# Kernel tuning notes

Measured on AMD Instinct MI355X. Metric: run time of the kernel, lower is better.

The kernel has to match this reference:

```python
import jax, jax.numpy as jnp
import numpy as np

MODEL_DIM = 1024
TOTAL_DIM = 1024
N_HEADS = 16
HEAD_DIM = TOTAL_DIM // N_HEADS


def setup_inputs() -> dict:
    key = jax.random.key(0)
    k1, k2, k3 = jax.random.split(key, 3)
    query = jax.random.normal(k1, (2, 2048, MODEL_DIM), dtype=jnp.float32)
    # nn.Linear(model_dim, 3*total_dim, bias=False): store as [in, out] for x @ W
    W_in = jax.random.normal(k2, (MODEL_DIM, 3 * TOTAL_DIM), dtype=jnp.float32) / np.sqrt(MODEL_DIM)
    W_out = jax.random.normal(k3, (TOTAL_DIM, MODEL_DIM), dtype=jnp.float32) / np.sqrt(TOTAL_DIM)
    return {"query": query, "W_in": W_in, "W_out": W_out}


def reference(query, W_in, W_out):
    B, S, _ = query.shape
    qkv = query @ W_in                      # [B, S, 3*D]
    q, k, v = jnp.split(qkv, 3, axis=-1)    # each [B, S, D]

    def to_heads(t):
        return t.reshape(B, S, N_HEADS, HEAD_DIM).transpose(0, 2, 1, 3)  # [B,H,S,d]

    q, k, v = to_heads(q), to_heads(k), to_heads(v)
    scale = 1.0 / np.sqrt(HEAD_DIM).astype(np.float32)
    scores = jnp.einsum('bhqd,bhkd->bhqk', q, k) * scale  # [B,H,S,S]
    causal = jnp.tril(jnp.ones((S, S), dtype=bool))
    scores = jnp.where(causal, scores, jnp.finfo(scores.dtype).min)
    probs = jax.nn.softmax(scores, axis=-1)
    attn = jnp.einsum('bhqk,bhkd->bhqd', probs, v)        # [B,H,S,d]
    attn = attn.transpose(0, 2, 1, 3).reshape(B, S, TOTAL_DIM)
    return attn @ W_out                     # [B, S, model_dim]
```

## Files before the change

### kernel.cpp

```cpp
#include <hip/hip_runtime.h>


typedef __bf16 bf16x8 __attribute__((ext_vector_type(8)));
typedef float f32x4 __attribute__((ext_vector_type(4)));
typedef int i32x4 __attribute__((ext_vector_type(4)));

#define B_   2
#define S_   2048
#define DM   1024
#define NH   16
#define HD   64
#define N3   3072
#define M_   4096

#define SCALE_LOG2E 0.180336884f

__device__ __forceinline__ unsigned short f2bf(float f) {
  unsigned int u = __float_as_uint(f);
  u += 0x7fffu + ((u >> 16) & 1u);
  return (unsigned short)(u >> 16);
}

__device__ __forceinline__ void gload_lds16(void* lds, const void* g) {
  __builtin_amdgcn_global_load_lds(
      (__attribute__((address_space(1))) void*)g,
      (__attribute__((address_space(3))) void*)lds, 16, 0, 0);
}

__global__ __launch_bounds__(256) void f32_to_bf16_vec(
    const float4* __restrict__ in, unsigned short* __restrict__ out, int n4) {
  int i = blockIdx.x * 256 + threadIdx.x;
  if (i < n4) {
    float4 v = in[i];
    ushort4 o;
    o.x = f2bf(v.x); o.y = f2bf(v.y); o.z = f2bf(v.z); o.w = f2bf(v.w);
    *(ushort4*)(&out[(size_t)i * 4]) = o;
  }
}

__global__ __launch_bounds__(256) void transpose_f32_bf16(
    const float* __restrict__ in, unsigned short* __restrict__ out, int R, int C) {
  __shared__ float tile[32][33];
  const int tx = threadIdx.x, ty = threadIdx.y;
  const int x = blockIdx.x * 32 + tx;
  const int y0 = blockIdx.y * 32;
#pragma unroll
  for (int j = 0; j < 32; j += 8)
    tile[ty + j][tx] = in[(size_t)(y0 + ty + j) * C + x];
  __syncthreads();
  const int ox = y0 + tx;
  const int oy0 = blockIdx.x * 32;
#pragma unroll
  for (int j = 0; j < 32; j += 8)
    out[(size_t)(oy0 + ty + j) * R + ox] = f2bf(tile[tx][ty + j]);
}

__global__ __launch_bounds__(256) void transpose_v(
    const unsigned short* __restrict__ qkv, unsigned short* __restrict__ vT) {
  __shared__ unsigned short tile[32][33];
  const int tx = threadIdx.x, ty = threadIdx.y;
  const int c0 = blockIdx.x * 32;
  const int r0 = blockIdx.y * 32;
#pragma unroll
  for (int j = 0; j < 32; j += 8)
    tile[ty + j][tx] = qkv[(size_t)(r0 + ty + j) * N3 + 2 * DM + c0 + tx];
  __syncthreads();
  const int b = r0 >> 11;
  const int srow = (r0 & 2047);
  const int head = c0 >> 6;
#pragma unroll
  for (int j = 0; j < 32; j += 8) {
    const int d = (c0 & 63) + ty + j;
    vT[(size_t)((b * NH + head) * HD + d) * S_ + srow + tx] = tile[tx][ty + j];
  }
}

template <int OUT_BF16>
__global__ __launch_bounds__(256) void gemm_abt(
    const unsigned short* __restrict__ A, const unsigned short* __restrict__ Bt,
    void* __restrict__ Cv, int M, int N, int K) {
  __shared__ __align__(16) unsigned short a_sm[128 * 32];
  __shared__ __align__(16) unsigned short b_sm[128 * 32];
  const int tid = threadIdx.x;
  const int lane = tid & 63, wave = tid >> 6;
  const int quad = lane >> 4, l15 = lane & 15;
  const int row0 = blockIdx.y * 128, col0 = blockIdx.x * 128;
  const int wm = (wave >> 1) * 64, wn = (wave & 1) * 64;

  f32x4 acc[4][4];
#pragma unroll
  for (int i = 0; i < 4; i++)
#pragma unroll
    for (int j = 0; j < 4; j++) acc[i][j] = (f32x4){0.f, 0.f, 0.f, 0.f};

  const int e0 = tid * 8;

  for (int k0 = 0; k0 < K; k0 += 32) {
    __syncthreads();
#pragma unroll
    for (int i = 0; i < 2; i++) {
      int e = e0 + i * 2048;
      int r = e >> 5, c = e & 31;
      gload_lds16(&a_sm[e], &A[(size_t)(row0 + r) * K + k0 + c]);
      gload_lds16(&b_sm[e], &Bt[(size_t)(col0 + r) * K + k0 + c]);
    }
    __syncthreads();

    bf16x8 af[4], bfb[4];
#pragma unroll
    for (int i = 0; i < 4; i++) {
      af[i]  = *(const bf16x8*)&a_sm[(wm + i * 16 + l15) * 32 + quad * 8];
      bfb[i] = *(const bf16x8*)&b_sm[(wn + i * 16 + l15) * 32 + quad * 8];
    }
#pragma unroll
    for (int i = 0; i < 4; i++)
#pragma unroll
      for (int j = 0; j < 4; j++)
        acc[i][j] = __builtin_amdgcn_mfma_f32_16x16x32_bf16(af[i], bfb[j], acc[i][j], 0, 0, 0);
  }

#pragma unroll
  for (int i = 0; i < 4; i++) {
#pragma unroll
    for (int j = 0; j < 4; j++) {
#pragma unroll
      for (int r = 0; r < 4; r++) {
        const int row = row0 + wm + i * 16 + quad * 4 + r;
        const int col = col0 + wn + j * 16 + l15;
        const float v = acc[i][j][r];
        if (OUT_BF16)
          ((unsigned short*)Cv)[(size_t)row * N + col] = f2bf(v);
        else
          ((float*)Cv)[(size_t)row * N + col] = v;
      }
    }
  }
}

__global__ __launch_bounds__(512, 4) void attn_fused3(
    const unsigned short* __restrict__ qkv,
    const unsigned short* __restrict__ vT,
    unsigned short* __restrict__ attnout) {
  const int h = blockIdx.y, b = blockIdx.z;
  const int qt = (b == 0) ? blockIdx.x : (15 - blockIdx.x);
  const int tid = threadIdx.x;
  const int lane = tid & 63, wave = tid >> 6;
  const int quad = lane >> 4, l15 = lane & 15;
  const int sw = l15 & 7;

  __shared__ __align__(16) unsigned short k_sm[2 * 4096];
  __shared__ __align__(16) unsigned short vt_sm[2 * 4096];

  const int Q0 = qt * 128;
  const int qrow = Q0 + wave * 16 + l15;
  const int wrow0 = Q0 + wave * 16;

  bf16x8 qf[2];
  {
    const unsigned short* qp = qkv + (size_t)(b * S_ + qrow) * N3 + h * HD + quad * 8;
    qf[0] = *(const bf16x8*)qp;
    qf[1] = *(const bf16x8*)(qp + 32);
  }

  f32x4 o[4];
#pragma unroll
  for (int n = 0; n < 4; n++) o[n] = (f32x4){0.f, 0.f, 0.f, 0.f};
  float lsum = 0.f;

  const int r0s = tid >> 3;
  const int gch = ((tid & 7) ^ (r0s & 7)) * 8;
  const unsigned short* kgb = qkv + (size_t)(b * S_ + r0s) * N3 + DM + h * HD + gch;
  const unsigned short* vgb = vT + (size_t)((b * NH + h) * HD + r0s) * S_ + gch;

  const int addrA = (((quad * 2) & 3) * 16 + l15) * 4;
  const int addrB = (((quad * 2 + 1) & 3) * 16 + l15) * 4;

  const int nt = 2 * qt + 2;
  gload_lds16(&k_sm[tid * 8], kgb);
  gload_lds16(&vt_sm[tid * 8], vgb);

  for (int t = 0; t < nt; t++) {
    __syncthreads();
    if (t + 1 < nt) {
      const int nb = ((t + 1) & 1) * 4096;
      gload_lds16(&k_sm[nb + tid * 8], kgb + (size_t)(t + 1) * 64 * N3);
      gload_lds16(&vt_sm[nb + tid * 8], vgb + (t + 1) * 64);
    }
    if (t * 64 > wrow0 + 15) continue;

    const unsigned short* kb = &k_sm[(t & 1) * 4096];
    const unsigned short* vb = &vt_sm[(t & 1) * 4096];

    f32x4 s[4];
#pragma unroll
    for (int mb = 0; mb < 4; mb++) s[mb] = (f32x4){0.f, 0.f, 0.f, 0.f};
#pragma unroll
    for (int mb = 0; mb < 4; mb++) {
      const int ro = (mb * 16 + l15) * 64;
      bf16x8 kf0 = *(const bf16x8*)&kb[ro + ((quad ^ sw) << 3)];
      bf16x8 kf1 = *(const bf16x8*)&kb[ro + (((4 + quad) ^ sw) << 3)];
      s[mb] = __builtin_amdgcn_mfma_f32_16x16x32_bf16(kf0, qf[0], s[mb], 0, 0, 0);
      s[mb] = __builtin_amdgcn_mfma_f32_16x16x32_bf16(kf1, qf[1], s[mb], 0, 0, 0);
    }

    if (t * 64 + 63 <= wrow0) {
#pragma unroll
      for (int mb = 0; mb < 4; mb++)
#pragma unroll
        for (int r = 0; r < 4; r++)
          s[mb][r] = exp2f(s[mb][r] * SCALE_LOG2E);
    } else {
      const int kb0 = t * 64 + quad * 4;
#pragma unroll
      for (int mb = 0; mb < 4; mb++)
#pragma unroll
        for (int r = 0; r < 4; r++) {
          const float e = exp2f(s[mb][r] * SCALE_LOG2E);
          s[mb][r] = (kb0 + mb * 16 + r <= qrow) ? e : 0.f;
        }
    }
#pragma unroll
    for (int mb = 0; mb < 4; mb++)
      lsum += (s[mb][0] + s[mb][1]) + (s[mb][2] + s[mb][3]);

    int pk[4][2];
#pragma unroll
    for (int mb = 0; mb < 4; mb++) {
      const unsigned u0 = __float_as_uint(s[mb][0]) + 0x8000u;
      const unsigned u1 = __float_as_uint(s[mb][1]) + 0x8000u;
      const unsigned u2 = __float_as_uint(s[mb][2]) + 0x8000u;
      const unsigned u3 = __float_as_uint(s[mb][3]) + 0x8000u;
      pk[mb][0] = (int)__builtin_amdgcn_perm(u1, u0, 0x07060302u);
      pk[mb][1] = (int)__builtin_amdgcn_perm(u3, u2, 0x07060302u);
    }

    const bool hi = quad >= 2;
#pragma unroll
    for (int ks = 0; ks < 2; ks++) {
      const int m0 = 2 * ks, m1 = m0 + 1;
      const int f0a = __builtin_amdgcn_ds_bpermute(addrA, pk[m0][0]);
      const int f0b = __builtin_amdgcn_ds_bpermute(addrA, pk[m1][0]);
      const int f1a = __builtin_amdgcn_ds_bpermute(addrA, pk[m0][1]);
      const int f1b = __builtin_amdgcn_ds_bpermute(addrA, pk[m1][1]);
      const int f2a = __builtin_amdgcn_ds_bpermute(addrB, pk[m0][0]);
      const int f2b = __builtin_amdgcn_ds_bpermute(addrB, pk[m1][0]);
      const int f3a = __builtin_amdgcn_ds_bpermute(addrB, pk[m0][1]);
      const int f3b = __builtin_amdgcn_ds_bpermute(addrB, pk[m1][1]);
      i32x4 fr;
      fr.x = hi ? f0b : f0a;
      fr.y = hi ? f1b : f1a;
      fr.z = hi ? f2b : f2a;
      fr.w = hi ? f3b : f3a;
      const bf16x8 pfrag = __builtin_bit_cast(bf16x8, fr);
#pragma unroll
      for (int mb = 0; mb < 4; mb++) {
        const int ro = (mb * 16 + l15) * 64;
        bf16x8 vf = *(const bf16x8*)&vb[ro + (((ks * 4 + quad) ^ sw) << 3)];
        o[mb] = __builtin_amdgcn_mfma_f32_16x16x32_bf16(vf, pfrag, o[mb], 0, 0, 0);
      }
    }
  }

  float l = lsum;
  l += __shfl_xor(l, 16);
  l += __shfl_xor(l, 32);
  const float inv = 1.0f / l;
  const size_t grow = (size_t)(b * S_ + qrow);
#pragma unroll
  for (int mb = 0; mb < 4; mb++) {
    ushort4 w;
    w.x = f2bf(o[mb][0] * inv);
    w.y = f2bf(o[mb][1] * inv);
    w.z = f2bf(o[mb][2] * inv);
    w.w = f2bf(o[mb][3] * inv);
    *(ushort4*)&attnout[grow * DM + h * HD + mb * 16 + quad * 4] = w;
  }
}

extern "C" void kernel_launch(void* const* d_in, const int* in_sizes, int n_in,
                              void* d_out, int out_size, void* d_ws, size_t ws_size,
                              hipStream_t stream) {
  const float* query = (const float*)d_in[0];
  const float* w_in  = (const float*)d_in[1];
  const float* w_out = (const float*)d_in[2];
  float* out = (float*)d_out;

  char* ws = (char*)d_ws;
  unsigned short* qbf     = (unsigned short*)(ws);
  unsigned short* vT      = (unsigned short*)(ws);
  unsigned short* w_in_t  = (unsigned short*)(ws + 8388608);
  unsigned short* w_out_t = (unsigned short*)(ws + 14680064);
  unsigned short* qkv     = (unsigned short*)(ws + 16777216);
  unsigned short* attn    = (unsigned short*)(ws + 41943040);

  f32_to_bf16_vec<<<dim3(M_ * DM / 1024), dim3(256), 0, stream>>>(
      (const float4*)query, qbf, M_ * DM / 4);
  transpose_f32_bf16<<<dim3(N3 / 32, DM / 32), dim3(32, 8), 0, stream>>>(w_in, w_in_t, DM, N3);
  transpose_f32_bf16<<<dim3(DM / 32, DM / 32), dim3(32, 8), 0, stream>>>(w_out, w_out_t, DM, DM);
  gemm_abt<1><<<dim3(N3 / 128, M_ / 128), dim3(256), 0, stream>>>(qbf, w_in_t, qkv, M_, N3, DM);
  transpose_v<<<dim3(DM / 32, M_ / 32), dim3(32, 8), 0, stream>>>(qkv, vT);
  attn_fused3<<<dim3(S_ / 128, NH, B_), dim3(512), 0, stream>>>(qkv, vT, attn);
  gemm_abt<0><<<dim3(DM / 128, M_ / 128), dim3(256), 0, stream>>>(attn, w_out_t, out, M_, DM, DM);
}
```

Baseline: 203.5 us.

## Fuse V transpose into QKV GEMM, shrink attention tiles, retile output GEMM

The QKV projection GEMM now writes Q/K into a 2048-wide buffer and emits V directly in transposed per-head layout by swapping MFMA operands, which removes the separate transpose_v kernel. It also uses a K-step of 64 with XOR-swizzled LDS and an XCD-aware block-to-tile mapping. Attention moves to 256-thread blocks over 64-row query tiles, which doubles the grid and drops the per-wave causal skip. The output GEMM gets a 128x64 tile for more blocks. The changes target a kernel launch, extra traffic for V, and low occupancy, at the cost of more K/V reloads in attention.

```diff
diff --git a/kernel.cpp b/kernel.cpp
--- a/kernel.cpp
+++ b/kernel.cpp
@@ -55,109 +55,123 @@
     out[(size_t)(oy0 + ty + j) * R + ox] = f2bf(tile[tx][ty + j]);
 }
 
-__global__ __launch_bounds__(256) void transpose_v(
-    const unsigned short* __restrict__ qkv, unsigned short* __restrict__ vT) {
-  __shared__ unsigned short tile[32][33];
-  const int tx = threadIdx.x, ty = threadIdx.y;
-  const int c0 = blockIdx.x * 32;
-  const int r0 = blockIdx.y * 32;
-#pragma unroll
-  for (int j = 0; j < 32; j += 8)
-    tile[ty + j][tx] = qkv[(size_t)(r0 + ty + j) * N3 + 2 * DM + c0 + tx];
-  __syncthreads();
-  const int b = r0 >> 11;
-  const int srow = (r0 & 2047);
-  const int head = c0 >> 6;
-#pragma unroll
-  for (int j = 0; j < 32; j += 8) {
-    const int d = (c0 & 63) + ty + j;
-    vT[(size_t)((b * NH + head) * HD + d) * S_ + srow + tx] = tile[tx][ty + j];
-  }
-}
-
-template <int OUT_BF16>
-__global__ __launch_bounds__(256) void gemm_abt(
-    const unsigned short* __restrict__ A, const unsigned short* __restrict__ Bt,
-    void* __restrict__ Cv, int M, int N, int K) {
-  __shared__ __align__(16) unsigned short a_sm[128 * 32];
-  __shared__ __align__(16) unsigned short b_sm[128 * 32];
-  const int tid = threadIdx.x;
-  const int lane = tid & 63, wave = tid >> 6;
-  const int quad = lane >> 4, l15 = lane & 15;
-  const int row0 = blockIdx.y * 128, col0 = blockIdx.x * 128;
-  const int wm = (wave >> 1) * 64, wn = (wave & 1) * 64;
-
-  f32x4 acc[4][4];
-#pragma unroll
-  for (int i = 0; i < 4; i++)
-#pragma unroll
-    for (int j = 0; j < 4; j++) acc[i][j] = (f32x4){0.f, 0.f, 0.f, 0.f};
-
-  const int e0 = tid * 8;
-
-  for (int k0 = 0; k0 < K; k0 += 32) {
-    __syncthreads();
-#pragma unroll
-    for (int i = 0; i < 2; i++) {
-      int e = e0 + i * 2048;
-      int r = e >> 5, c = e & 31;
-      gload_lds16(&a_sm[e], &A[(size_t)(row0 + r) * K + k0 + c]);
-      gload_lds16(&b_sm[e], &Bt[(size_t)(col0 + r) * K + k0 + c]);
-    }
-    __syncthreads();
-
-    bf16x8 af[4], bfb[4];
-#pragma unroll
-    for (int i = 0; i < 4; i++) {
-      af[i]  = *(const bf16x8*)&a_sm[(wm + i * 16 + l15) * 32 + quad * 8];
-      bfb[i] = *(const bf16x8*)&b_sm[(wn + i * 16 + l15) * 32 + quad * 8];
-    }
-#pragma unroll
-    for (int i = 0; i < 4; i++)
-#pragma unroll
-      for (int j = 0; j < 4; j++)
-        acc[i][j] = __builtin_amdgcn_mfma_f32_16x16x32_bf16(af[i], bfb[j], acc[i][j], 0, 0, 0);
-  }
-
-#pragma unroll
-  for (int i = 0; i < 4; i++) {
-#pragma unroll
-    for (int j = 0; j < 4; j++) {
-#pragma unroll
-      for (int r = 0; r < 4; r++) {
-        const int row = row0 + wm + i * 16 + quad * 4 + r;
-        const int col = col0 + wn + j * 16 + l15;
-        const float v = acc[i][j][r];
-        if (OUT_BF16)
-          ((unsigned short*)Cv)[(size_t)row * N + col] = f2bf(v);
-        else
-          ((float*)Cv)[(size_t)row * N + col] = v;
-      }
-    }
-  }
-}
-
-__global__ __launch_bounds__(512, 4) void attn_fused3(
-    const unsigned short* __restrict__ qkv,
-    const unsigned short* __restrict__ vT,
-    unsigned short* __restrict__ attnout) {
-  const int h = blockIdx.y, b = blockIdx.z;
-  const int qt = (b == 0) ? blockIdx.x : (15 - blockIdx.x);
+__global__ __launch_bounds__(256) void gemm_qkv(
+    const unsigned short* __restrict__ A,
+    const unsigned short* __restrict__ Bt,
+    unsigned short* __restrict__ qkv2,
+    unsigned short* __restrict__ vT) {
+  __shared__ __align__(16) unsigned short a_sm[128 * 64];
+  __shared__ __align__(16) unsigned short b_sm[128 * 64];
+  const int id = blockIdx.x;
+  const int xcd = id & 7, j8 = id >> 3;
+  const int ct = xcd * 3 + (j8 % 3);
+  const int rt = j8 / 3;
+  const bool isv = ct >= 16;
+  const int row0 = rt * 128, col0 = ct * 128;
+
   const int tid = threadIdx.x;
   const int lane = tid & 63, wave = tid >> 6;
   const int quad = lane >> 4, l15 = lane & 15;
   const int sw = l15 & 7;
+  const int wm = (wave >> 1) * 64, wn = (wave & 1) * 64;
+
+  f32x4 acc[4][4];
+#pragma unroll
+  for (int i = 0; i < 4; i++)
+#pragma unroll
+    for (int j = 0; j < 4; j++) acc[i][j] = (f32x4){0.f, 0.f, 0.f, 0.f};
+
+  const int c_src = ((tid & 7) ^ ((tid >> 3) & 7)) * 8;
+  const int r_st = tid >> 3;
+  const unsigned short* Ab = A + (size_t)(row0 + r_st) * DM + c_src;
+  const unsigned short* Bb = Bt + (size_t)(col0 + r_st) * DM + c_src;
+
+  for (int k0 = 0; k0 < DM; k0 += 64) {
+    __syncthreads();
+#pragma unroll
+    for (int rnd = 0; rnd < 4; rnd++) {
+      gload_lds16(&a_sm[tid * 8 + rnd * 2048], Ab + k0 + (size_t)rnd * 32 * DM);
+      gload_lds16(&b_sm[tid * 8 + rnd * 2048], Bb + k0 + (size_t)rnd * 32 * DM);
+    }
+    __syncthreads();
+
+    bf16x8 af[4][2], bfr[4][2];
+#pragma unroll
+    for (int i = 0; i < 4; i++)
+#pragma unroll
+      for (int h = 0; h < 2; h++) {
+        const int ch = ((h * 4 + quad) ^ sw) << 3;
+        af[i][h]  = *(const bf16x8*)&a_sm[(wm + i * 16 + l15) * 64 + ch];
+        bfr[i][h] = *(const bf16x8*)&b_sm[(wn + i * 16 + l15) * 64 + ch];
+      }
+    if (!isv) {
+#pragma unroll
+      for (int i = 0; i < 4; i++)
+#pragma unroll
+        for (int j = 0; j < 4; j++)
+#pragma unroll
+          for (int h = 0; h < 2; h++)
+            acc[i][j] = __builtin_amdgcn_mfma_f32_16x16x32_bf16(af[i][h], bfr[j][h], acc[i][j], 0, 0, 0);
+    } else {
+#pragma unroll
+      for (int i = 0; i < 4; i++)
+#pragma unroll
+        for (int j = 0; j < 4; j++)
+#pragma unroll
+          for (int h = 0; h < 2; h++)
+            acc[i][j] = __builtin_amdgcn_mfma_f32_16x16x32_bf16(bfr[i][h], af[j][h], acc[i][j], 0, 0, 0);
+    }
+  }
+
+  if (!isv) {
+#pragma unroll
+    for (int i = 0; i < 4; i++)
+#pragma unroll
+      for (int j = 0; j < 4; j++)
+#pragma unroll
+        for (int r = 0; r < 4; r++) {
+          const int row = row0 + wm + i * 16 + quad * 4 + r;
+          const int col = col0 + wn + j * 16 + l15;
+          qkv2[(size_t)row * 2048 + col] = f2bf(acc[i][j][r]);
+        }
+  } else {
+    const int head = ((col0 - 2048) >> 6) + (wn >> 6);
+    const int bidx = row0 >> 11;
+    const int s_base = (row0 & 2047) + wm;
+#pragma unroll
+    for (int i = 0; i < 4; i++)
+#pragma unroll
+      for (int j = 0; j < 4; j++)
+#pragma unroll
+        for (int r = 0; r < 4; r++) {
+          const int d = i * 16 + quad * 4 + r;
+          const int s = s_base + j * 16 + l15;
+          vT[((size_t)((bidx * NH + head) * HD + d)) * S_ + s] = f2bf(acc[i][j][r]);
+        }
+  }
+}
+
+__global__ __launch_bounds__(256) void attn_fused4(
+    const unsigned short* __restrict__ qkv2,
+    const unsigned short* __restrict__ vT,
+    unsigned short* __restrict__ attnout) {
+  const int h = blockIdx.y, b = blockIdx.z;
+  const int qt = (b == 0) ? blockIdx.x : (31 - blockIdx.x);
+  const int tid = threadIdx.x;
+  const int lane = tid & 63, wave = tid >> 6;
+  const int quad = lane >> 4, l15 = lane & 15;
+  const int sw = l15 & 7;
 
   __shared__ __align__(16) unsigned short k_sm[2 * 4096];
   __shared__ __align__(16) unsigned short vt_sm[2 * 4096];
 
-  const int Q0 = qt * 128;
+  const int Q0 = qt * 64;
   const int qrow = Q0 + wave * 16 + l15;
   const int wrow0 = Q0 + wave * 16;
 
   bf16x8 qf[2];
   {
-    const unsigned short* qp = qkv + (size_t)(b * S_ + qrow) * N3 + h * HD + quad * 8;
+    const unsigned short* qp = qkv2 + (size_t)(b * S_ + qrow) * 2048 + h * HD + quad * 8;
     qf[0] = *(const bf16x8*)qp;
     qf[1] = *(const bf16x8*)(qp + 32);
   }
@@ -169,24 +183,29 @@
 
   const int r0s = tid >> 3;
   const int gch = ((tid & 7) ^ (r0s & 7)) * 8;
-  const unsigned short* kgb = qkv + (size_t)(b * S_ + r0s) * N3 + DM + h * HD + gch;
+  const unsigned short* kgb = qkv2 + (size_t)(b * S_ + r0s) * 2048 + DM + h * HD + gch;
   const unsigned short* vgb = vT + (size_t)((b * NH + h) * HD + r0s) * S_ + gch;
 
   const int addrA = (((quad * 2) & 3) * 16 + l15) * 4;
   const int addrB = (((quad * 2 + 1) & 3) * 16 + l15) * 4;
 
-  const int nt = 2 * qt + 2;
+  const int nt = qt + 1;
   gload_lds16(&k_sm[tid * 8], kgb);
+  gload_lds16(&k_sm[2048 + tid * 8], kgb + (size_t)32 * 2048);
   gload_lds16(&vt_sm[tid * 8], vgb);
+  gload_lds16(&vt_sm[2048 + tid * 8], vgb + (size_t)32 * S_);
 
   for (int t = 0; t < nt; t++) {
     __syncthreads();
     if (t + 1 < nt) {
       const int nb = ((t + 1) & 1) * 4096;
-      gload_lds16(&k_sm[nb + tid * 8], kgb + (size_t)(t + 1) * 64 * N3);
-      gload_lds16(&vt_sm[nb + tid * 8], vgb + (t + 1) * 64);
-    }
-    if (t * 64 > wrow0 + 15) continue;
+      const unsigned short* kg = kgb + (size_t)(t + 1) * 64 * 2048;
+      const unsigned short* vg = vgb + (t + 1) * 64;
+      gload_lds16(&k_sm[nb + tid * 8], kg);
+      gload_lds16(&k_sm[nb + 2048 + tid * 8], kg + (size_t)32 * 2048);
+      gload_lds16(&vt_sm[nb + tid * 8], vg);
+      gload_lds16(&vt_sm[nb + 2048 + tid * 8], vg + (size_t)32 * S_);
+    }
 
     const unsigned short* kb = &k_sm[(t & 1) * 4096];
     const unsigned short* vb = &vt_sm[(t & 1) * 4096];
@@ -203,7 +222,7 @@
       s[mb] = __builtin_amdgcn_mfma_f32_16x16x32_bf16(kf1, qf[1], s[mb], 0, 0, 0);
     }
 
-    if (t * 64 + 63 <= wrow0) {
+    if (t < qt) {
 #pragma unroll
       for (int mb = 0; mb < 4; mb++)
 #pragma unroll
@@ -277,6 +296,62 @@
   }
 }
 
+__global__ __launch_bounds__(256) void gemm_out(
+    const unsigned short* __restrict__ A,
+    const unsigned short* __restrict__ Bt,
+    float* __restrict__ C) {
+  __shared__ __align__(16) unsigned short a_sm[128 * 32];
+  __shared__ __align__(16) unsigned short b_sm[64 * 32];
+  const int id = blockIdx.x;
+  const int ctile = id & 15, rtile = id >> 4;
+  const int row0 = rtile * 128, col0 = ctile * 64;
+
+  const int tid = threadIdx.x;
+  const int lane = tid & 63, wave = tid >> 6;
+  const int quad = lane >> 4, l15 = lane & 15;
+  const int wm = wave * 32;
+
+  f32x4 acc[2][4];
+#pragma unroll
+  for (int i = 0; i < 2; i++)
+#pragma unroll
+    for (int j = 0; j < 4; j++) acc[i][j] = (f32x4){0.f, 0.f, 0.f, 0.f};
+
+  const int rA = tid >> 2, cA = (tid & 3) * 8;
+
+  for (int k0 = 0; k0 < DM; k0 += 32) {
+    __syncthreads();
+    gload_lds16(&a_sm[tid * 8],        &A[(size_t)(row0 + rA) * DM + k0 + cA]);
+    gload_lds16(&a_sm[tid * 8 + 2048], &A[(size_t)(row0 + rA + 64) * DM + k0 + cA]);
+    gload_lds16(&b_sm[tid * 8],        &Bt[(size_t)(col0 + rA) * DM + k0 + cA]);
+    __syncthreads();
+
+    bf16x8 af[2], bf[4];
+#pragma unroll
+    for (int i = 0; i < 2; i++)
+      af[i] = *(const bf16x8*)&a_sm[(wm + i * 16 + l15) * 32 + quad * 8];
+#pragma unroll
+    for (int j = 0; j < 4; j++)
+      bf[j] = *(const bf16x8*)&b_sm[(j * 16 + l15) * 32 + quad * 8];
+#pragma unroll
+    for (int i = 0; i < 2; i++)
+#pragma unroll
+      for (int j = 0; j < 4; j++)
+        acc[i][j] = __builtin_amdgcn_mfma_f32_16x16x32_bf16(af[i], bf[j], acc[i][j], 0, 0, 0);
+  }
+
+#pragma unroll
+  for (int i = 0; i < 2; i++)
+#pragma unroll
+    for (int j = 0; j < 4; j++)
+#pragma unroll
+      for (int r = 0; r < 4; r++) {
+        const int row = row0 + wm + i * 16 + quad * 4 + r;
+        const int col = col0 + j * 16 + l15;
+        C[(size_t)row * DM + col] = acc[i][j][r];
+      }
+}
+
 extern "C" void kernel_launch(void* const* d_in, const int* in_sizes, int n_in,
                               void* d_out, int out_size, void* d_ws, size_t ws_size,
                               hipStream_t stream) {
@@ -287,18 +362,17 @@
 
   char* ws = (char*)d_ws;
   unsigned short* qbf     = (unsigned short*)(ws);
-  unsigned short* vT      = (unsigned short*)(ws);
   unsigned short* w_in_t  = (unsigned short*)(ws + 8388608);
   unsigned short* w_out_t = (unsigned short*)(ws + 14680064);
-  unsigned short* qkv     = (unsigned short*)(ws + 16777216);
+  unsigned short* qkv2    = (unsigned short*)(ws + 16777216);
+  unsigned short* vT      = (unsigned short*)(ws + 33554432);
   unsigned short* attn    = (unsigned short*)(ws + 41943040);
 
   f32_to_bf16_vec<<<dim3(M_ * DM / 1024), dim3(256), 0, stream>>>(
       (const float4*)query, qbf, M_ * DM / 4);
   transpose_f32_bf16<<<dim3(N3 / 32, DM / 32), dim3(32, 8), 0, stream>>>(w_in, w_in_t, DM, N3);
   transpose_f32_bf16<<<dim3(DM / 32, DM / 32), dim3(32, 8), 0, stream>>>(w_out, w_out_t, DM, DM);
-  gemm_abt<1><<<dim3(N3 / 128, M_ / 128), dim3(256), 0, stream>>>(qbf, w_in_t, qkv, M_, N3, DM);
-  transpose_v<<<dim3(DM / 32, M_ / 32), dim3(32, 8), 0, stream>>>(qkv, vT);
-  attn_fused3<<<dim3(S_ / 128, NH, B_), dim3(512), 0, stream>>>(qkv, vT, attn);
-  gemm_abt<0><<<dim3(DM / 128, M_ / 128), dim3(256), 0, stream>>>(attn, w_out_t, out, M_, DM, DM);
-}
+  gemm_qkv<<<dim3(768), dim3(256), 0, stream>>>(qbf, w_in_t, qkv2, vT);
+  attn_fused4<<<dim3(32, NH, B_), dim3(256), 0, stream>>>(qkv2, vT, attn);
+  gemm_out<<<dim3(512), dim3(256), 0, stream>>>(attn, w_out_t, out);
+}
```

Result: slower. 215.2 us (+5.7%).
